# Kernel optimization log

Measured on AMD Instinct MI355X. Metric: run time of the kernel, lower is better.

Reference implementation:

```python
import jax, jax.numpy as jnp
import numpy as np
from jax.scipy.linalg import expm

H = 4096      # h_dim
U = 3072      # u_dim = 3*32*32
D = 1024      # d_dim
Y = 1024      # y_dim
DELTA = 0.1


def setup_inputs() -> dict:
    key = jax.random.key(0)
    k0, k1, k2, k3, k4, k5 = jax.random.split(key, 6)
    bw = 1.0 / np.sqrt(H)
    bb = 1.0 / np.sqrt(U + D)
    W_w = jax.random.uniform(k0, (H, H), jnp.float32, -bw, bw)
    B_w = jax.random.uniform(k1, (H, U + D), jnp.float32, -bb, bb)
    C_w = jax.random.uniform(k2, (Y, H), jnp.float32, -bw, bw)
    h = jax.random.normal(k3, (1, H), jnp.float32)
    u = jax.random.normal(k4, (1, U), jnp.float32)
    du = jax.random.normal(k5, (1, D), jnp.float32)
    return {"u": u, "du": du, "h": h, "W_w": W_w, "B_w": B_w, "C_w": C_w}


def reference(u, du, h, W_w, B_w, C_w):
    # Antisymmetric part of W
    A = 0.5 * (W_w - W_w.T)                      # [H,H], skew-symmetric
    A_expm = expm(A * DELTA)                     # [H,H]
    # rec = F.linear(h, A_expm) = h @ A_expm^T
    rec = h @ A_expm.T                           # [1,H]
    # B(cat([du, u], dim=1))
    udu = jnp.concatenate([du, u], axis=1)       # [1, D+U]
    b = udu @ B_w.T                              # [1,H]
    # inp = A^{-1} (expm(A*delta) - I) b
    A_inv = jnp.linalg.inv(A)
    M = A_inv @ (A_expm - jnp.eye(H, dtype=A.dtype))  # [H,H]
    inp = (M @ b[..., None])[..., 0]             # [1,H]
    h_new = rec + inp                            # [1,H]
    # sigma is identity; y = C(h_new)
    y = h_new @ C_w.T                            # [1,Y]
    return y
```

## Files before the change

kernel.cpp:

```cpp
#include <hip/hip_runtime.h>


#define Hd 4096
#define Dd 1024
#define DELTA 0.1f
#define NSTEP 3

using u16 = unsigned short;
using u32 = unsigned int;

__device__ __forceinline__ float blo(u32 p){ return __uint_as_float(p << 16); }
__device__ __forceinline__ float bhi(u32 p){ return __uint_as_float(p & 0xFFFF0000u); }
__device__ __forceinline__ u16 f2bf(float f){
  u32 u = __float_as_uint(f);
  u32 r = (u + 0x7FFFu + ((u >> 16) & 1u)) >> 16;
  return (u16)r;
}
__device__ __forceinline__ float wred(float x){
  #pragma unroll
  for (int off = 32; off > 0; off >>= 1) x += __shfl_down(x, off, 64);
  return x;
}
__device__ __forceinline__ float dot8(uint4 a, const float* v){
  float s;
  s  = blo(a.x)*v[0] + bhi(a.x)*v[1];
  s += blo(a.y)*v[2] + bhi(a.y)*v[3];
  s += blo(a.z)*v[4] + bhi(a.z)*v[5];
  s += blo(a.w)*v[6] + bhi(a.w)*v[7];
  return s;
}

__global__ __launch_bounds__(256) void prep_kernel(const float* __restrict__ W,
                                                   const float* __restrict__ Bw,
                                                   const float* __restrict__ uu,
                                                   const float* __restrict__ du,
                                                   const float* __restrict__ h,
                                                   u16* __restrict__ A,
                                                   float* __restrict__ v0, float* __restrict__ w0,
                                                   float* __restrict__ rec, float* __restrict__ inp){
  __shared__ float T1[64][68];
  __shared__ float T2[64][68];
  const int tid = threadIdx.x;
  const int bj = blockIdx.x, bi = blockIdx.y;
  if (bi <= bj){
    const int rb = bi * 64, cb = bj * 64;
    #pragma unroll
    for (int q = 0; q < 4; q++){
      int ch = q*256 + tid;
      int r = ch >> 4, c4 = (ch & 15) << 2;
      *(float4*)(&T1[r][c4]) = *(const float4*)(W + (size_t)(rb + r)*Hd + cb + c4);
      *(float4*)(&T2[r][c4]) = *(const float4*)(W + (size_t)(cb + r)*Hd + rb + c4);
    }
    __syncthreads();
    #pragma unroll
    for (int q = 0; q < 2; q++){
      int ch = q*256 + tid;
      int r = ch >> 3, c8 = (ch & 7) << 3;
      union { u16 s[8]; uint4 v; } o1, o2;
      #pragma unroll
      for (int j = 0; j < 8; j++){
        int c = c8 + j;
        o1.s[j] = f2bf(0.5f*(T1[r][c] - T2[c][r]));
        o2.s[j] = f2bf(0.5f*(T2[r][c] - T1[c][r]));
      }
      *(uint4*)(A + (size_t)(rb + r)*Hd + cb + c8) = o1.v;
      *(uint4*)(A + (size_t)(cb + r)*Hd + rb + c8) = o2.v;
    }
  } else {
    const int t = (bi*(bi-1))/2 + bj;
    if (t >= 1024) return;
    const int lane = tid & 63, wave = tid >> 6;
    const int row = t*4 + wave;
    const float* Br = Bw + (size_t)row * Hd;
    float acc = 0.f;
    #pragma unroll
    for (int it = 0; it < 16; it++){
      int c = it*256 + lane*4;
      float4 a = *(const float4*)(Br + c);
      const float* src = (c < Dd) ? (du + c) : (uu + (c - Dd));
      float4 x = *(const float4*)src;
      acc += a.x*x.x + a.y*x.y + a.z*x.z + a.w*x.w;
    }
    acc = wred(acc);
    if (lane == 0){ float val = DELTA * acc; w0[row] = val; inp[row] = val; }
    if (tid < 4){ int e = t*4 + tid; float hv = h[e]; v0[e] = hv; rec[e] = hv; }
  }
}

__global__ __launch_bounds__(256) void step_kernel(const u16* __restrict__ A,
                                                   const float* __restrict__ vin,
                                                   const float* __restrict__ win,
                                                   float* __restrict__ vout, float* __restrict__ wout,
                                                   float* __restrict__ rec, float* __restrict__ inp,
                                                   float cv, float cw){
  __shared__ float sv[Hd], sw[Hd];
  const int tid = threadIdx.x;
  for (int i = tid; i < Hd/4; i += 256){
    ((float4*)sv)[i] = ((const float4*)vin)[i];
    ((float4*)sw)[i] = ((const float4*)win)[i];
  }
  __syncthreads();
  const int lane = tid & 63, wave = tid >> 6;
  const int row0 = blockIdx.x*8 + wave*2;
  const u16* A0 = A + (size_t)row0 * Hd;
  const u16* A1 = A0 + Hd;
  float av0 = 0, aw0 = 0, av1 = 0, aw1 = 0;
  #pragma unroll
  for (int it = 0; it < 8; it++){
    int c = it*512 + lane*8;
    uint4 a0 = *(const uint4*)(A0 + c);
    uint4 a1 = *(const uint4*)(A1 + c);
    const float* vv = sv + c;
    const float* ww = sw + c;
    av0 += dot8(a0, vv); aw0 += dot8(a0, ww);
    av1 += dot8(a1, vv); aw1 += dot8(a1, ww);
  }
  av0 = wred(av0); aw0 = wred(aw0); av1 = wred(av1); aw1 = wred(aw1);
  if (lane == 0){
    float nv0 = cv*av0, nw0 = cw*aw0;
    vout[row0]   = nv0; rec[row0]   += nv0;
    wout[row0]   = nw0; inp[row0]   += nw0;
    float nv1 = cv*av1, nw1 = cw*aw1;
    vout[row0+1] = nv1; rec[row0+1] += nv1;
    wout[row0+1] = nw1; inp[row0+1] += nw1;
  }
}

__global__ __launch_bounds__(256) void c_kernel(const float* __restrict__ Cw,
                                                const float* __restrict__ rec,
                                                const float* __restrict__ inp,
                                                float* __restrict__ y){
  __shared__ float hn[Hd];
  const int tid = threadIdx.x;
  for (int i = tid; i < Hd/4; i += 256){
    float4 r4 = ((const float4*)rec)[i];
    float4 i4 = ((const float4*)inp)[i];
    float4 s; s.x = r4.x+i4.x; s.y = r4.y+i4.y; s.z = r4.z+i4.z; s.w = r4.w+i4.w;
    ((float4*)hn)[i] = s;
  }
  __syncthreads();
  const int lane = tid & 63, wave = tid >> 6;
  const int row = blockIdx.x*4 + wave;
  const float* Cr = Cw + (size_t)row * Hd;
  float acc = 0.f;
  #pragma unroll
  for (int it = 0; it < 16; it++){
    int c = it*256 + lane*4;
    float4 a = *(const float4*)(Cr + c);
    acc += a.x*hn[c] + a.y*hn[c+1] + a.z*hn[c+2] + a.w*hn[c+3];
  }
  acc = wred(acc);
  if (lane == 0) y[row] = acc;
}

extern "C" void kernel_launch(void* const* d_in, const int* in_sizes, int n_in,
                              void* d_out, int out_size, void* d_ws, size_t ws_size,
                              hipStream_t stream){
  const float* uu = (const float*)d_in[0];
  const float* du = (const float*)d_in[1];
  const float* h  = (const float*)d_in[2];
  const float* W  = (const float*)d_in[3];
  const float* Bw = (const float*)d_in[4];
  const float* Cw = (const float*)d_in[5];
  float* y = (float*)d_out;

  char* ws = (char*)d_ws;
  u16* A = (u16*)ws;
  float* fbase = (float*)(ws + (size_t)Hd * Hd * sizeof(u16));
  float* vb[2] = { fbase,        fbase +   Hd };
  float* wb[2] = { fbase + 2*Hd, fbase + 3*Hd };
  float* rec   = fbase + 4*Hd;
  float* inp   = fbase + 5*Hd;

  prep_kernel<<<dim3(64, 64), 256, 0, stream>>>(W, Bw, uu, du, h, A,
                                                vb[0], wb[0], rec, inp);
  for (int k = 0; k < NSTEP; k++){
    step_kernel<<<512, 256, 0, stream>>>(A, vb[k & 1], wb[k & 1],
                                         vb[(k + 1) & 1], wb[(k + 1) & 1],
                                         rec, inp,
                                         DELTA / (float)(k + 1), DELTA / (float)(k + 2));
  }
  c_kernel<<<256, 256, 0, stream>>>(Cw, rec, inp, y);
}
```

Before: 195.7 us.

## Cut Taylor series to two steps and restructure skew-symmetric prep tiling

Result: no change. 192.6 us (-1.6%).

```diff
diff --git a/kernel.cpp b/kernel.cpp
--- a/kernel.cpp
+++ b/kernel.cpp
@@ -4,7 +4,6 @@
 #define Hd 4096
 #define Dd 1024
 #define DELTA 0.1f
-#define NSTEP 3
 
 using u16 = unsigned short;
 using u32 = unsigned int;
@@ -38,37 +37,38 @@
                                                    u16* __restrict__ A,
                                                    float* __restrict__ v0, float* __restrict__ w0,
                                                    float* __restrict__ rec, float* __restrict__ inp){
-  __shared__ float T1[64][68];
-  __shared__ float T2[64][68];
+  __shared__ float S[64 * 65];
   const int tid = threadIdx.x;
-  const int bj = blockIdx.x, bi = blockIdx.y;
-  if (bi <= bj){
-    const int rb = bi * 64, cb = bj * 64;
+  const int b = blockIdx.x;
+  if (b < 4096){
+    const int bi = b >> 6, bj = b & 63;
+    const float* Wt = W + (size_t)(bj * 64) * Hd + bi * 64;
     #pragma unroll
     for (int q = 0; q < 4; q++){
       int ch = q*256 + tid;
       int r = ch >> 4, c4 = (ch & 15) << 2;
-      *(float4*)(&T1[r][c4]) = *(const float4*)(W + (size_t)(rb + r)*Hd + cb + c4);
-      *(float4*)(&T2[r][c4]) = *(const float4*)(W + (size_t)(cb + r)*Hd + rb + c4);
+      float4 t = *(const float4*)(Wt + (size_t)r * Hd + c4);
+      float* d = S + r*65 + c4;
+      d[0] = t.x; d[1] = t.y; d[2] = t.z; d[3] = t.w;
     }
     __syncthreads();
+    const float* Wr = W + (size_t)(bi * 64) * Hd + bj * 64;
+    u16* Ar = A + (size_t)(bi * 64) * Hd + bj * 64;
     #pragma unroll
     for (int q = 0; q < 2; q++){
       int ch = q*256 + tid;
       int r = ch >> 3, c8 = (ch & 7) << 3;
-      union { u16 s[8]; uint4 v; } o1, o2;
+      float4 t0 = *(const float4*)(Wr + (size_t)r * Hd + c8);
+      float4 t1 = *(const float4*)(Wr + (size_t)r * Hd + c8 + 4);
+      float tt[8] = { t0.x,t0.y,t0.z,t0.w, t1.x,t1.y,t1.z,t1.w };
+      union { u16 s[8]; uint4 v; } o;
       #pragma unroll
-      for (int j = 0; j < 8; j++){
-        int c = c8 + j;
-        o1.s[j] = f2bf(0.5f*(T1[r][c] - T2[c][r]));
-        o2.s[j] = f2bf(0.5f*(T2[r][c] - T1[c][r]));
-      }
-      *(uint4*)(A + (size_t)(rb + r)*Hd + cb + c8) = o1.v;
-      *(uint4*)(A + (size_t)(cb + r)*Hd + rb + c8) = o2.v;
+      for (int j = 0; j < 8; j++)
+        o.s[j] = f2bf(0.5f * (tt[j] - S[(c8 + j)*65 + r]));
+      *(uint4*)(Ar + (size_t)r * Hd + c8) = o.v;
     }
   } else {
-    const int t = (bi*(bi-1))/2 + bj;
-    if (t >= 1024) return;
+    const int t = b - 4096;
     const int lane = tid & 63, wave = tid >> 6;
     const int row = t*4 + wave;
     const float* Br = Bw + (size_t)row * Hd;
@@ -83,7 +83,7 @@
     }
     acc = wred(acc);
     if (lane == 0){ float val = DELTA * acc; w0[row] = val; inp[row] = val; }
-    if (tid < 4){ int e = t*4 + tid; float hv = h[e]; v0[e] = hv; rec[e] = hv; }
+    if (t < 16){ int e = t*256 + tid; float hv = h[e]; v0[e] = hv; rec[e] = hv; }
   }
 }
 
@@ -172,13 +172,10 @@
   float* rec   = fbase + 4*Hd;
   float* inp   = fbase + 5*Hd;
 
-  prep_kernel<<<dim3(64, 64), 256, 0, stream>>>(W, Bw, uu, du, h, A,
-                                                vb[0], wb[0], rec, inp);
-  for (int k = 0; k < NSTEP; k++){
-    step_kernel<<<512, 256, 0, stream>>>(A, vb[k & 1], wb[k & 1],
-                                         vb[(k + 1) & 1], wb[(k + 1) & 1],
-                                         rec, inp,
-                                         DELTA / (float)(k + 1), DELTA / (float)(k + 2));
-  }
+  prep_kernel<<<5120, 256, 0, stream>>>(W, Bw, uu, du, h, A, vb[0], wb[0], rec, inp);
+  step_kernel<<<512, 256, 0, stream>>>(A, vb[0], wb[0], vb[1], wb[1], rec, inp,
+                                       DELTA / 1.0f, DELTA / 2.0f);
+  step_kernel<<<512, 256, 0, stream>>>(A, vb[1], wb[1], vb[0], wb[0], rec, inp,
+                                       DELTA / 2.0f, DELTA / 3.0f);
   c_kernel<<<256, 256, 0, stream>>>(Cw, rec, inp, y);
 }
```
